# Kernel tuning notes

Hardware: AMD Instinct MI355X
Metric: run time of the kernel (lower is better)

## Reference

```python
import jax, jax.numpy as jnp
import numpy as np

N = 50000          # nodes
E = 800000         # edges (before self-loops)
DIN = 1024         # input_dim_mel
HID = 128          # hidden_dim
HEADS = 2
NC = 4             # num_classes
NEG_SLOPE = 0.2    # PyG GATConv default


def setup_inputs() -> dict:
    key = jax.random.key(0)
    ks = jax.random.split(key, 12)
    s = 0.05
    return {
        "x": jax.random.normal(ks[0], (N, DIN), dtype=jnp.float32),
        "edge_index": jax.random.randint(ks[1], (2, E), 0, N, dtype=jnp.int64),
        # linear_pre (stored as [in, out])
        "W_pre": jax.random.normal(ks[2], (DIN, HID), dtype=jnp.float32) * s,
        "b_pre": jnp.zeros((HID,), dtype=jnp.float32),
        # gat1: GATConv(HID, HID, heads=2, concat=True)
        "W1": jax.random.normal(ks[3], (HID, HEADS * HID), dtype=jnp.float32) * s,
        "a_src1": jax.random.normal(ks[4], (HEADS, HID), dtype=jnp.float32) * s,
        "a_dst1": jax.random.normal(ks[5], (HEADS, HID), dtype=jnp.float32) * s,
        "b1": jnp.zeros((HEADS * HID,), dtype=jnp.float32),
        # gat2: GATConv(HID*HEADS, NC, heads=1, concat=True)
        "W2": jax.random.normal(ks[6], (HEADS * HID, NC), dtype=jnp.float32) * s,
        "a_src2": jax.random.normal(ks[7], (1, NC), dtype=jnp.float32) * s,
        "a_dst2": jax.random.normal(ks[8], (1, NC), dtype=jnp.float32) * s,
        "b2": jnp.zeros((NC,), dtype=jnp.float32),
    }


def _gat_conv(x, W, a_src, a_dst, bias, src, dst, heads, out_ch):
    """PyG GATConv (concat=True, self-loops already appended to src/dst)."""
    n = x.shape[0]
    h = (x @ W).reshape(n, heads, out_ch)            # [N,H,C]
    alpha_src = (h * a_src).sum(-1)                  # [N,H]
    alpha_dst = (h * a_dst).sum(-1)                  # [N,H]
    e = alpha_src[src] + alpha_dst[dst]              # [E,H] edge scores
    e = jax.nn.leaky_relu(e, NEG_SLOPE)
    # segment softmax over incoming edges of each dst node
    m = jax.ops.segment_max(e, dst, num_segments=n)  # [N,H]
    e = jnp.exp(e - m[dst])
    s = jax.ops.segment_sum(e, dst, num_segments=n)  # [N,H]
    alpha = e / (s[dst] + 1e-16)                     # [E,H]
    # gather src messages, weight by attention, scatter-add to dst
    out = jax.ops.segment_sum(h[src] * alpha[:, :, None], dst, num_segments=n)
    return out.reshape(n, heads * out_ch) + bias


def reference(x, edge_index, W_pre, b_pre, W1, a_src1, a_dst1, b1,
              W2, a_src2, a_dst2, b2):
    n = x.shape[0]
    # add self-loops (PyG GATConv default)
    loops = jnp.arange(n, dtype=edge_index.dtype)
    src = jnp.concatenate([edge_index[0], loops])
    dst = jnp.concatenate([edge_index[1], loops])

    h = jax.nn.relu(x @ W_pre + b_pre)                               # [N,HID]
    h = jax.nn.elu(_gat_conv(h, W1, a_src1, a_dst1, b1, src, dst, HEADS, HID))
    out = _gat_conv(h, W2, a_src2, a_dst2, b2, src, dst, 1, NC)      # [N,NC]
    return out
```

## Files before the change

kernel.cpp:

```cpp
#include <hip/hip_runtime.h>
#include <hip/hip_bf16.h>

#define NEG_SLOPE 0.2f

typedef _Float16 f16x8 __attribute__((ext_vector_type(8)));
typedef float f32x4 __attribute__((ext_vector_type(4)));
typedef unsigned short ushort_t;

#define AS_GLOBAL(p) ((const __attribute__((address_space(1))) void*)(p))
#define AS_SHARED(p) ((__attribute__((address_space(3))) void*)(p))


__global__ void khist(const int* __restrict__ dst, int E, int* __restrict__ counts) {
    int i = blockIdx.x * blockDim.x + threadIdx.x;
    if (i < E) atomicAdd(&counts[dst[i]], 1);
}

__global__ __launch_bounds__(1024) void kscan_part(const int* __restrict__ counts,
                                                   int* __restrict__ row_ptr,
                                                   int* __restrict__ bsum, int n) {
    __shared__ int wsum[16];
    int t = threadIdx.x, lane = t & 63, wid = t >> 6;
    int i = blockIdx.x * 1024 + t;
    int v = (i < n) ? (counts[i] + 1) : 0;
    int x = v;
    #pragma unroll
    for (int off = 1; off < 64; off <<= 1) {
        int y = __shfl_up(x, off, 64);
        if (lane >= off) x += y;
    }
    if (lane == 63) wsum[wid] = x;
    __syncthreads();
    if (wid == 0) {
        int ws = (lane < 16) ? wsum[lane] : 0;
        #pragma unroll
        for (int off = 1; off < 16; off <<= 1) {
            int y = __shfl_up(ws, off, 64);
            if (lane >= off) ws += y;
        }
        if (lane < 16) wsum[lane] = ws;
    }
    __syncthreads();
    int wave_excl = (wid == 0) ? 0 : wsum[wid - 1];
    if (i < n) row_ptr[i] = wave_excl + (x - v);
    if (t == 0) bsum[blockIdx.x] = wsum[15];
}

__global__ void kscan_tops(const int* __restrict__ bsum, int* __restrict__ boff,
                           int* __restrict__ row_ptr, int G, int n) {
    int lane = threadIdx.x;
    int v = (lane < G) ? bsum[lane] : 0;
    int x = v;
    #pragma unroll
    for (int off = 1; off < 64; off <<= 1) {
        int y = __shfl_up(x, off, 64);
        if (lane >= off) x += y;
    }
    if (lane < G) boff[lane] = x - v;
    if (lane == 63) row_ptr[n] = x;
}

__global__ void kscan_add(int* __restrict__ row_ptr, const int* __restrict__ boff,
                          int* __restrict__ cursor, int n) {
    int i = blockIdx.x * blockDim.x + threadIdx.x;
    if (i < n) {
        int r = row_ptr[i] + boff[i >> 10];
        row_ptr[i] = r;
        cursor[i] = r;
    }
}

__global__ void kfill(const int* __restrict__ src, const int* __restrict__ dst,
                      int E, int n, int* __restrict__ cursor, int* __restrict__ edge_src) {
    int i = blockIdx.x * blockDim.x + threadIdx.x;
    if (i < E) {
        int p = atomicAdd(&cursor[dst[i]], 1);
        edge_src[p] = src[i];
    } else if (i < E + n) {
        int v = i - E;
        int p = atomicAdd(&cursor[v], 1);
        edge_src[p] = v;
    }
}

__global__ void kprep(const float* __restrict__ Wpre, const float* __restrict__ W1,
                      ushort_t* __restrict__ PreF, ushort_t* __restrict__ W1h) {
    int i = blockIdx.x * blockDim.x + threadIdx.x;
    if (i < 1024 * 128) {
        int k = i >> 7, n = i & 127;
        int d = ((k >> 3) * 128 + n) * 8 + (k & 7);
        PreF[d] = __builtin_bit_cast(ushort_t, (_Float16)Wpre[i]);
    } else if (i < 1024 * 128 + 128 * 256) {
        int j2 = i - 1024 * 128;
        int k = j2 >> 8, n = j2 & 255;
        int d = ((k >> 3) * 256 + n) * 8 + (k & 7);
        W1h[d] = __builtin_bit_cast(ushort_t, (_Float16)W1[j2]);
    }
}

__device__ inline f16x8 cvt8(const float* v) {
    f16x8 r;
    #pragma unroll
    for (int i = 0; i < 8; ++i) r[i] = (_Float16)v[i];
    return r;
}

__global__ __launch_bounds__(256) void kgemm_mfma1(const float* __restrict__ A,
                                                   const ushort_t* __restrict__ Bf,
                                                   const float* __restrict__ bias,
                                                   ushort_t* __restrict__ C, int M) {
    __shared__ __align__(16) ushort_t Bs[8192];
    int t = threadIdx.x;
    int wid = t >> 6, lane = t & 63;
    int q = lane >> 4, l15 = lane & 15;
    int m0 = blockIdx.x * 64 + wid * 16;
    int m = m0 + l15;
    const float* arow = A + (size_t)(m < M ? m : 0) * 1024;

    f32x4 acc[8];
    #pragma unroll
    for (int c = 0; c < 8; ++c) acc[c] = (f32x4){0.f, 0.f, 0.f, 0.f};

    float4 av[2][4];
    #pragma unroll
    for (int ks = 0; ks < 2; ++ks) {
        av[0][ks * 2]     = *(const float4*)(arow + ks * 32 + q * 8);
        av[0][ks * 2 + 1] = *(const float4*)(arow + ks * 32 + q * 8 + 4);
    }

    #pragma unroll 2
    for (int kt = 0; kt < 16; ++kt) {
        int cur = kt & 1, nxt = cur ^ 1;
        __syncthreads();
        {
            const ushort_t* sF = Bf + kt * 8192;
            #pragma unroll
            for (int i = 0; i < 4; ++i) {
                int ge = (i * 256 + t) * 8;
                int le = (i * 256 + (t & 0xC0)) * 8;
                __builtin_amdgcn_global_load_lds(AS_GLOBAL(sF + ge), AS_SHARED(Bs + le), 16, 0, 0);
            }
        }
        if (kt < 15) {
            const float* a2 = arow + (kt + 1) * 64;
            #pragma unroll
            for (int ks = 0; ks < 2; ++ks) {
                av[nxt][ks * 2]     = *(const float4*)(a2 + ks * 32 + q * 8);
                av[nxt][ks * 2 + 1] = *(const float4*)(a2 + ks * 32 + q * 8 + 4);
            }
        }
        __syncthreads();
        #pragma unroll
        for (int ks = 0; ks < 2; ++ks) {
            f16x8 af = cvt8((const float*)&av[cur][ks * 2]);
            int kc = ks * 4 + q;
            #pragma unroll
            for (int c = 0; c < 8; ++c) {
                f16x8 b = *(const f16x8*)(Bs + (kc * 128 + c * 16 + l15) * 8);
                acc[c] = __builtin_amdgcn_mfma_f32_16x16x32_f16(af, b, acc[c], 0, 0, 0);
            }
        }
    }
    #pragma unroll
    for (int c = 0; c < 8; ++c) {
        int n = c * 16 + l15;
        float bv = bias[n];
        #pragma unroll
        for (int r = 0; r < 4; ++r) {
            int mm = m0 + q * 4 + r;
            if (mm < M)
                C[(size_t)mm * 128 + n] =
                    __builtin_bit_cast(ushort_t, (_Float16)fmaxf(acc[c][r] + bv, 0.f));
        }
    }
}

__global__ __launch_bounds__(256) void kgemm_mfma2(const ushort_t* __restrict__ Ah,
                                                   const ushort_t* __restrict__ W1h,
                                                   const float* __restrict__ a_src,
                                                   const float* __restrict__ a_dst,
                                                   ushort_t* __restrict__ C,
                                                   float* __restrict__ as1,
                                                   float* __restrict__ ad1, int M) {
    __shared__ __align__(16) ushort_t Bs[16384];
    int t = threadIdx.x;
    int wid = t >> 6, lane = t & 63;
    int q = lane >> 4, l15 = lane & 15;
    int g = blockIdx.y;
    int m0 = blockIdx.x * 64 + wid * 16;
    int m = m0 + l15;
    const ushort_t* arow = Ah + (size_t)(m < M ? m : 0) * 128;

    {
        #pragma unroll
        for (int i = 0; i < 8; ++i) {
            int j = i * 4 + wid;
            int kc = j >> 1, hk = j & 1;
            int ge = ((kc * 256) + g * 128 + hk * 64 + lane) * 8;
            int le = j * 512;
            __builtin_amdgcn_global_load_lds(AS_GLOBAL(W1h + ge), AS_SHARED(Bs + le), 16, 0, 0);
        }
    }
    f16x8 af[4];
    #pragma unroll
    for (int ks = 0; ks < 4; ++ks)
        af[ks] = *(const f16x8*)(arow + ks * 32 + q * 8);
    __syncthreads();

    f32x4 acc[8];
    #pragma unroll
    for (int c = 0; c < 8; ++c) acc[c] = (f32x4){0.f, 0.f, 0.f, 0.f};

    #pragma unroll
    for (int ks = 0; ks < 4; ++ks) {
        int kc = ks * 4 + q;
        #pragma unroll
        for (int c = 0; c < 8; ++c) {
            f16x8 b = *(const f16x8*)(Bs + (kc * 128 + c * 16 + l15) * 8);
            acc[c] = __builtin_amdgcn_mfma_f32_16x16x32_f16(af[ks], b, acc[c], 0, 0, 0);
        }
    }
    #pragma unroll
    for (int c = 0; c < 8; ++c) {
        int n = g * 128 + c * 16 + l15;
        #pragma unroll
        for (int r = 0; r < 4; ++r) {
            int mm = m0 + q * 4 + r;
            if (mm < M)
                C[(size_t)mm * 256 + n] = __builtin_bit_cast(ushort_t, (_Float16)acc[c][r]);
        }
    }
    float asv[4] = {0.f, 0.f, 0.f, 0.f};
    float adv[4] = {0.f, 0.f, 0.f, 0.f};
    #pragma unroll
    for (int c = 0; c < 8; ++c) {
        float sa = a_src[g * 128 + c * 16 + l15];
        float da = a_dst[g * 128 + c * 16 + l15];
        #pragma unroll
        for (int r = 0; r < 4; ++r) {
            asv[r] += acc[c][r] * sa;
            adv[r] += acc[c][r] * da;
        }
    }
    #pragma unroll
    for (int off = 1; off <= 8; off <<= 1) {
        #pragma unroll
        for (int r = 0; r < 4; ++r) {
            asv[r] += __shfl_xor(asv[r], off, 64);
            adv[r] += __shfl_xor(adv[r], off, 64);
        }
    }
    if (l15 == 0) {
        #pragma unroll
        for (int r = 0; r < 4; ++r) {
            int node = m0 + q * 4 + r;
            if (node < M) {
                as1[node * 2 + g] = asv[r];
                ad1[node * 2 + g] = adv[r];
            }
        }
    }
}

__global__ __launch_bounds__(128) void kagg1(const ushort_t* __restrict__ h1h,
                                             const float* __restrict__ as1,
                                             const float* __restrict__ ad1,
                                             const float* __restrict__ b1,
                                             const float* __restrict__ W2,
                                             const float* __restrict__ a_src2,
                                             const float* __restrict__ a_dst2,
                                             const int* __restrict__ row_ptr,
                                             const int* __restrict__ edge_src,
                                             float* __restrict__ h2,
                                             float* __restrict__ as2,
                                             float* __restrict__ ad2, int n) {
    __shared__ float w_lds[128];
    __shared__ int   s_lds[64];
    __shared__ float red[2][4];
    int node = blockIdx.x;
    int t = threadIdx.x;
    int wid = t >> 6;
    int beg = row_ptr[node], end = row_ptr[node + 1];
    int h_ch = t >> 6;
    float advv = ad1[node * 2 + (t & 1)];
    float acc0 = 0.f, acc1 = 0.f, ssum = 0.f;
    for (int base = beg; base < end; base += 64) {
        int cnt = min(64, end - base);
        int i = t >> 1, h = t & 1;
        if (i < cnt) {
            int s = edge_src[base + i];
            float e = as1[s * 2 + h] + advv;
            e = (e > 0.f) ? e : NEG_SLOPE * e;
            w_lds[i * 2 + h] = __expf(e);
            if (h == 0) s_lds[i] = s;
        }
        __syncthreads();
        #pragma unroll 4
        for (int i2 = 0; i2 < cnt; ++i2) {
            float wv = w_lds[i2 * 2 + h_ch];
            int s = s_lds[i2];
            unsigned p = *(const unsigned*)(h1h + (size_t)s * 256 + t * 2);
            _Float16 lo16 = __builtin_bit_cast(_Float16, (ushort_t)(p & 0xffffu));
            _Float16 hi16 = __builtin_bit_cast(_Float16, (ushort_t)(p >> 16));
            acc0 += wv * (float)lo16;
            acc1 += wv * (float)hi16;
            ssum += wv;
        }
        __syncthreads();
    }
    float inv = 1.f / (ssum + 1e-16f);
    float o0 = acc0 * inv + b1[t * 2];
    float o1 = acc1 * inv + b1[t * 2 + 1];
    o0 = (o0 > 0.f) ? o0 : (__expf(o0) - 1.f);
    o1 = (o1 > 0.f) ? o1 : (__expf(o1) - 1.f);
    float4 w0 = *(const float4*)(W2 + t * 8);
    float4 w1 = *(const float4*)(W2 + t * 8 + 4);
    float p0 = o0 * w0.x + o1 * w1.x;
    float p1 = o0 * w0.y + o1 * w1.y;
    float p2 = o0 * w0.z + o1 * w1.z;
    float p3 = o0 * w0.w + o1 * w1.w;
    #pragma unroll
    for (int off = 1; off < 64; off <<= 1) {
        p0 += __shfl_xor(p0, off, 64);
        p1 += __shfl_xor(p1, off, 64);
        p2 += __shfl_xor(p2, off, 64);
        p3 += __shfl_xor(p3, off, 64);
    }
    if ((t & 63) == 0) {
        red[wid][0] = p0; red[wid][1] = p1; red[wid][2] = p2; red[wid][3] = p3;
    }
    __syncthreads();
    if (t == 0) {
        float hv[4], s2 = 0.f, d2 = 0.f;
        #pragma unroll
        for (int j = 0; j < 4; ++j) {
            hv[j] = red[0][j] + red[1][j];
            h2[node * 4 + j] = hv[j];
            s2 += hv[j] * a_src2[j];
            d2 += hv[j] * a_dst2[j];
        }
        as2[node] = s2;
        ad2[node] = d2;
    }
}

__global__ __launch_bounds__(256) void kagg2(const float* __restrict__ h2,
                                             const float* __restrict__ as2,
                                             const float* __restrict__ ad2,
                                             const float* __restrict__ b2,
                                             const int* __restrict__ row_ptr,
                                             const int* __restrict__ edge_src,
                                             float* __restrict__ out, int n) {
    int wid = threadIdx.x >> 6, lane = threadIdx.x & 63;
    int node = blockIdx.x * 4 + wid;
    if (node >= n) return;
    int beg = row_ptr[node], end = row_ptr[node + 1];
    int j = lane & 3, ig = lane >> 2;
    float adv = ad2[node];
    float acc = 0.f, ssum = 0.f;
    for (int p = beg + ig; p < end; p += 16) {
        int s = edge_src[p];
        float e = as2[s] + adv;
        e = (e > 0.f) ? e : NEG_SLOPE * e;
        float wv = __expf(e);
        acc += wv * h2[s * 4 + j];
        ssum += wv;
    }
    #pragma unroll
    for (int off = 32; off >= 4; off >>= 1) {
        acc += __shfl_down(acc, off);
        ssum += __shfl_down(ssum, off);
    }
    if (lane < 4) out[node * 4 + j] = acc / (ssum + 1e-16f) + b2[j];
}

extern "C" void kernel_launch(void* const* d_in, const int* in_sizes, int n_in,
                              void* d_out, int out_size, void* d_ws, size_t ws_size,
                              hipStream_t stream) {
    const float* x      = (const float*)d_in[0];
    const int*   ei     = (const int*)d_in[1];
    const float* W_pre  = (const float*)d_in[2];
    const float* b_pre  = (const float*)d_in[3];
    const float* W1     = (const float*)d_in[4];
    const float* a_src1 = (const float*)d_in[5];
    const float* a_dst1 = (const float*)d_in[6];
    const float* b1     = (const float*)d_in[7];
    const float* W2     = (const float*)d_in[8];
    const float* a_src2 = (const float*)d_in[9];
    const float* a_dst2 = (const float*)d_in[10];
    const float* b2     = (const float*)d_in[11];
    float* out = (float*)d_out;

    const int DIN = 1024;
    const int E = in_sizes[1] / 2;
    const int N = in_sizes[0] / DIN;

    const int* esrc = ei;
    const int* edst = ei + E;

    char* ws = (char*)d_ws;
    size_t off = 0;
    ushort_t* h1h = (ushort_t*)(ws + off); off += (size_t)N * 256 * 2;
    ushort_t* h0h = (ushort_t*)(ws + off); off += (size_t)N * 128 * 2;
    float* as1 = (float*)(ws + off);  off += (size_t)N * 2 * 4;
    float* ad1 = (float*)(ws + off);  off += (size_t)N * 2 * 4;
    float* h2  = (float*)(ws + off);  off += (size_t)N * 4 * 4;
    float* as2 = (float*)(ws + off);  off += (size_t)N * 4;
    float* ad2 = (float*)(ws + off);  off += (size_t)N * 4;
    int* row_ptr = (int*)(ws + off);  off += ((size_t)N + 16) * 4;
    int* cursor  = (int*)(ws + off);  off += (size_t)N * 4;
    int* counts  = (int*)(ws + off);  off += (size_t)N * 4;
    int* bsum    = (int*)(ws + off);  off += 64 * 4;
    int* boff    = (int*)(ws + off);  off += 64 * 4;
    int* edge_src = (int*)(ws + off); off += (size_t)(E + N) * 4;
    ushort_t* PreF = (ushort_t*)(ws + off); off += 1024 * 128 * 2;
    ushort_t* W1h  = (ushort_t*)(ws + off); off += 128 * 256 * 2;

    int G = (N + 1023) / 1024;

    kprep<<<640, 256, 0, stream>>>(W_pre, W1, PreF, W1h);
    hipMemsetAsync(counts, 0, (size_t)N * 4, stream);
    khist<<<(E + 255) / 256, 256, 0, stream>>>(edst, E, counts);
    kscan_part<<<G, 1024, 0, stream>>>(counts, row_ptr, bsum, N);
    kscan_tops<<<1, 64, 0, stream>>>(bsum, boff, row_ptr, G, N);
    kscan_add<<<(N + 255) / 256, 256, 0, stream>>>(row_ptr, boff, cursor, N);
    kfill<<<(E + N + 255) / 256, 256, 0, stream>>>(esrc, edst, E, N, cursor, edge_src);

    int Mb = (N + 63) / 64;
    kgemm_mfma1<<<Mb, 256, 0, stream>>>(x, PreF, b_pre, h0h, N);
    {
        dim3 grid(Mb, 2);
        kgemm_mfma2<<<grid, 256, 0, stream>>>(h0h, W1h, a_src1, a_dst1, h1h, as1, ad1, N);
    }
    kagg1<<<N, 128, 0, stream>>>(h1h, as1, ad1, b1, W2, a_src2, a_dst2,
                                 row_ptr, edge_src, h2, as2, ad2, N);
    kagg2<<<(N + 3) / 4, 256, 0, stream>>>(h2, as2, ad2, b2, row_ptr, edge_src, out, N);
}
```

Measured before the change: 533.4 us.

## Retile first GEMM to 32-row blocks with swizzled LDS staging of A

The x@W_pre GEMM now uses 32-row blocks, with the 4 waves arranged 2x2 over rows and columns, so the grid doubles in size. A rows are loaded with coalesced row-contiguous float4 reads, converted to fp16, and stored in LDS with an XOR swizzle before MFMA fragments are read. The aim is more blocks in flight and better global coalescing on the 200MB fp32 read of x. In exchange, the shared W_pre tile is reloaded by twice as many blocks, and each iteration adds LDS writes for A.

```diff
diff --git a/kernel.cpp b/kernel.cpp
--- a/kernel.cpp
+++ b/kernel.cpp
@@ -4,6 +4,7 @@
 #define NEG_SLOPE 0.2f
 
 typedef _Float16 f16x8 __attribute__((ext_vector_type(8)));
+typedef _Float16 f16x4 __attribute__((ext_vector_type(4)));
 typedef float f32x4 __attribute__((ext_vector_type(4)));
 typedef unsigned short ushort_t;
 
@@ -98,10 +99,10 @@
     }
 }
 
-__device__ inline f16x8 cvt8(const float* v) {
-    f16x8 r;
-    #pragma unroll
-    for (int i = 0; i < 8; ++i) r[i] = (_Float16)v[i];
+__device__ inline f16x4 cvt4(float4 v) {
+    f16x4 r;
+    r[0] = (_Float16)v.x; r[1] = (_Float16)v.y;
+    r[2] = (_Float16)v.z; r[3] = (_Float16)v.w;
     return r;
 }
 
@@ -110,23 +111,30 @@
                                                    const float* __restrict__ bias,
                                                    ushort_t* __restrict__ C, int M) {
     __shared__ __align__(16) ushort_t Bs[8192];
+    __shared__ __align__(16) ushort_t As[2048];
     int t = threadIdx.x;
-    int wid = t >> 6, lane = t & 63;
-    int q = lane >> 4, l15 = lane & 15;
-    int m0 = blockIdx.x * 64 + wid * 16;
-    int m = m0 + l15;
-    const float* arow = A + (size_t)(m < M ? m : 0) * 1024;
-
-    f32x4 acc[8];
-    #pragma unroll
-    for (int c = 0; c < 8; ++c) acc[c] = (f32x4){0.f, 0.f, 0.f, 0.f};
-
-    float4 av[2][4];
-    #pragma unroll
-    for (int ks = 0; ks < 2; ++ks) {
-        av[0][ks * 2]     = *(const float4*)(arow + ks * 32 + q * 8);
-        av[0][ks * 2 + 1] = *(const float4*)(arow + ks * 32 + q * 8 + 4);
-    }
+    int wid = t >> 6, lane = t & 63, q = lane >> 4, l15 = lane & 15;
+    int wr = wid & 1, wc = wid >> 1;
+    int m0 = blockIdx.x * 32;
+
+    int ar = t >> 3, ac = t & 7;
+    int srow = m0 + ar;
+    if (srow >= M) srow = M - 1;
+    const float* sA = A + (size_t)srow * 1024;
+    int sw = ar & 7;
+    int wadr0 = ar * 64 + (((ac >> 1)) ^ sw) * 8 + (ac & 1) * 4;
+    int wadr1 = ar * 64 + ((4 + (ac >> 1)) ^ sw) * 8 + (ac & 1) * 4;
+
+    float4 av[2][2];
+    av[0][0] = *(const float4*)(sA + ac * 4);
+    av[0][1] = *(const float4*)(sA + 32 + ac * 4);
+
+    f32x4 acc[4];
+    #pragma unroll
+    for (int c = 0; c < 4; ++c) acc[c] = (f32x4){0.f, 0.f, 0.f, 0.f};
+
+    int arow_rd = (wr * 16 + l15) * 64;
+    int asw = l15 & 7;
 
     #pragma unroll 2
     for (int kt = 0; kt < 16; ++kt) {
@@ -142,32 +150,31 @@
             }
         }
         if (kt < 15) {
-            const float* a2 = arow + (kt + 1) * 64;
+            const float* a2 = sA + (kt + 1) * 64;
+            av[nxt][0] = *(const float4*)(a2 + ac * 4);
+            av[nxt][1] = *(const float4*)(a2 + 32 + ac * 4);
+        }
+        *(f16x4*)(As + wadr0) = cvt4(av[cur][0]);
+        *(f16x4*)(As + wadr1) = cvt4(av[cur][1]);
+        __syncthreads();
+        #pragma unroll
+        for (int ks = 0; ks < 2; ++ks) {
+            int kc = ks * 4 + q;
+            f16x8 af = *(const f16x8*)(As + arow_rd + ((kc ^ asw) * 8));
             #pragma unroll
-            for (int ks = 0; ks < 2; ++ks) {
-                av[nxt][ks * 2]     = *(const float4*)(a2 + ks * 32 + q * 8);
-                av[nxt][ks * 2 + 1] = *(const float4*)(a2 + ks * 32 + q * 8 + 4);
-            }
-        }
-        __syncthreads();
-        #pragma unroll
-        for (int ks = 0; ks < 2; ++ks) {
-            f16x8 af = cvt8((const float*)&av[cur][ks * 2]);
-            int kc = ks * 4 + q;
-            #pragma unroll
-            for (int c = 0; c < 8; ++c) {
-                f16x8 b = *(const f16x8*)(Bs + (kc * 128 + c * 16 + l15) * 8);
+            for (int c = 0; c < 4; ++c) {
+                f16x8 b = *(const f16x8*)(Bs + (kc * 128 + wc * 64 + c * 16 + l15) * 8);
                 acc[c] = __builtin_amdgcn_mfma_f32_16x16x32_f16(af, b, acc[c], 0, 0, 0);
             }
         }
     }
     #pragma unroll
-    for (int c = 0; c < 8; ++c) {
-        int n = c * 16 + l15;
+    for (int c = 0; c < 4; ++c) {
+        int n = wc * 64 + c * 16 + l15;
         float bv = bias[n];
         #pragma unroll
         for (int r = 0; r < 4; ++r) {
-            int mm = m0 + q * 4 + r;
+            int mm = m0 + wr * 16 + q * 4 + r;
             if (mm < M)
                 C[(size_t)mm * 128 + n] =
                     __builtin_bit_cast(ushort_t, (_Float16)fmaxf(acc[c][r] + bv, 0.f));
@@ -426,9 +433,10 @@
     kscan_add<<<(N + 255) / 256, 256, 0, stream>>>(row_ptr, boff, cursor, N);
     kfill<<<(E + N + 255) / 256, 256, 0, stream>>>(esrc, edst, E, N, cursor, edge_src);
 
-    int Mb = (N + 63) / 64;
-    kgemm_mfma1<<<Mb, 256, 0, stream>>>(x, PreF, b_pre, h0h, N);
+    int Mb32 = (N + 31) / 32;
+    kgemm_mfma1<<<Mb32, 256, 0, stream>>>(x, PreF, b_pre, h0h, N);
     {
+        int Mb = (N + 63) / 64;
         dim3 grid(Mb, 2);
         kgemm_mfma2<<<grid, 256, 0, stream>>>(h0h, W1h, a_src1, a_dst1, h1h, as1, ad1, N);
     }
```

After: 521.6 us. 2.2% less time.
